# Performance work log

Measured on AMD Instinct MI355X. Metric: run time of the kernel, lower is better.

## Reference

```python
import jax, jax.numpy as jnp
import numpy as np


def _lstm_layer(x, W_ih, W_hh, b_ih, b_hh):
    """Single LSTM layer, batch_first input x: (B, T, in). PyTorch gate order i,f,g,o.
    Returns (full hidden sequence (B,T,H), final hidden (B,H))."""
    B = x.shape[0]
    H = W_hh.shape[1]
    # Precompute input projections for all timesteps (one big GEMM).
    x_proj = jnp.einsum('bti,gi->btg', x, W_ih) + (b_ih + b_hh)  # (B, T, 4H)
    x_proj = jnp.swapaxes(x_proj, 0, 1)  # (T, B, 4H) for scan
    h0 = jnp.zeros((B, H), x.dtype)
    c0 = jnp.zeros((B, H), x.dtype)

    def step(carry, xt):
        h, c = carry
        gates = xt + h @ W_hh.T  # (B, 4H)
        i, f, g, o = jnp.split(gates, 4, axis=-1)
        i = jax.nn.sigmoid(i)
        f = jax.nn.sigmoid(f)
        g = jnp.tanh(g)
        o = jax.nn.sigmoid(o)
        c = f * c + i * g
        h = o * jnp.tanh(c)
        return (h, c), h

    (hT, cT), hs = jax.lax.scan(step, (h0, c0), x_proj)
    return jnp.swapaxes(hs, 0, 1), hT  # (B,T,H), (B,H)


def setup_inputs() -> dict:
    key = jax.random.key(0)
    ks = jax.random.split(key, 9)
    B, T, I, H = 512, 2048, 3, 64
    s = 1.0 / float(np.sqrt(H))  # PyTorch LSTM init: U(-1/sqrt(H), 1/sqrt(H))

    def u(k, shape):
        return jax.random.uniform(k, shape, jnp.float32, -s, s)

    return {
        'x': jax.random.normal(ks[0], (B, T, I), jnp.float32),
        'W_ih0': u(ks[1], (4 * H, I)),
        'W_hh0': u(ks[2], (4 * H, H)),
        'b_ih0': u(ks[3], (4 * H,)),
        'b_hh0': u(ks[4], (4 * H,)),
        'W_ih1': u(ks[5], (4 * H, H)),
        'W_hh1': u(ks[6], (4 * H, H)),
        'b_ih1': u(ks[7], (4 * H,)),
        'b_hh1': u(ks[8], (4 * H,)),
    }


def reference(x, W_ih0, W_hh0, b_ih0, b_hh0, W_ih1, W_hh1, b_ih1, b_hh1):
    # 2-layer LSTM; inter-layer dropout (p=0.2) is inactive in eval mode, so omitted
    # for deterministic correctness checking.
    h1_seq, _ = _lstm_layer(x, W_ih0, W_hh0, b_ih0, b_hh0)
    _, h2_final = _lstm_layer(h1_seq, W_ih1, W_hh1, b_ih1, b_hh1)
    return h2_final  # (B, H) == h_n[-1]
```

## Files before the change

kernel.cpp:

```cpp
#include <hip/hip_runtime.h>
#include <math.h>


typedef _Float16 half8 __attribute__((ext_vector_type(8)));
typedef float    f32x4 __attribute__((ext_vector_type(4)));

constexpr int TT = 2048;
constexpr int HSTR = 80;

#define LOG2E  1.44269504088896340736f
#define LOG2E2 2.88539008177792681472f

__device__ __forceinline__ float sig_p(float y) {
    return __builtin_amdgcn_rcpf(1.0f + __builtin_amdgcn_exp2f(-y));
}
__device__ __forceinline__ float tanh_p(float y) {
    return 1.0f - 2.0f * __builtin_amdgcn_rcpf(__builtin_amdgcn_exp2f(y) + 1.0f);
}
__device__ __forceinline__ float sel4(f32x4 v, int q) {
    float lo = (q & 1) ? v[1] : v[0];
    float hi = (q & 1) ? v[3] : v[2];
    return (q & 2) ? hi : lo;
}

__device__ __forceinline__ void lds_barrier() {
    __builtin_amdgcn_sched_barrier(0);
    asm volatile("s_waitcnt lgkmcnt(0)" ::: "memory");
    __builtin_amdgcn_s_barrier();
    __builtin_amdgcn_sched_barrier(0);
}

__global__ __launch_bounds__(512) void lstm2_fused(
    const float* __restrict__ x,
    const float* __restrict__ Wih0, const float* __restrict__ Whh0,
    const float* __restrict__ bih0, const float* __restrict__ bhh0,
    const float* __restrict__ Wih1, const float* __restrict__ Whh1,
    const float* __restrict__ bih1, const float* __restrict__ bhh1,
    float* __restrict__ out)
{
    __shared__ __align__(16) _Float16 h1a[2][4 * HSTR];
    __shared__ __align__(16) _Float16 h2a[2][4 * HSTR];

    const int tid  = threadIdx.x;
    const int lane = tid & 63;
    const int wid  = tid >> 6;
    const int quad = lane >> 4;
    const int l16  = lane & 15;
    const bool isL1 = (wid >= 4);
    const int col  = (wid & 3) * 16 + l16;

    for (int i = tid; i < 2 * 4 * HSTR; i += 512) {
        ((_Float16*)h1a)[i] = (_Float16)0.0f;
        ((_Float16*)h2a)[i] = (_Float16)0.0f;
    }

    half8 wA[4][2];
    half8 wB[4][2];
    f32x4 cbias[4];
    float wxa[4], wxb[4], wxc[4];
    #pragma unroll
    for (int c = 0; c < 4; ++c) {
        const int row = c * 64 + col;
        const float sc = (c == 2) ? LOG2E2 : LOG2E;
        if (!isL1) {
            #pragma unroll
            for (int f = 0; f < 2; ++f) {
                const float* p = Whh0 + (size_t)row * 64 + f * 32 + quad * 8;
                half8 h;
                #pragma unroll
                for (int u = 0; u < 8; ++u) h[u] = (_Float16)(p[u] * sc);
                wA[c][f] = h;
            }
            const float b = (bih0[row] + bhh0[row]) * sc;
            cbias[c] = f32x4{b, b, b, b};
            wxa[c] = Wih0[row*3+0] * sc;
            wxb[c] = Wih0[row*3+1] * sc;
            wxc[c] = Wih0[row*3+2] * sc;
        } else {
            #pragma unroll
            for (int f = 0; f < 2; ++f) {
                const float* p = Whh1 + (size_t)row * 64 + f * 32 + quad * 8;
                half8 h;
                #pragma unroll
                for (int u = 0; u < 8; ++u) h[u] = (_Float16)(p[u] * sc);
                wA[c][f] = h;
                const float* q = Wih1 + (size_t)row * 64 + f * 32 + quad * 8;
                half8 g;
                #pragma unroll
                for (int u = 0; u < 8; ++u) g[u] = (_Float16)(q[u] * sc);
                wB[c][f] = g;
            }
            const float b = (bih1[row] + bhh1[row]) * sc;
            cbias[c] = f32x4{b, b, b, b};
        }
    }

    const float* xq = x + (size_t)(blockIdx.x * 4 + quad) * TT * 3;
    float xn0 = 0.f, xn1 = 0.f, xn2 = 0.f;
    if (!isL1) { xn0 = xq[0]; xn1 = xq[1]; xn2 = xq[2]; }

    const f32x4 Z = {0.f, 0.f, 0.f, 0.f};
    float cst = 0.0f;

    f32x4 accQ[2][4];
    #pragma unroll
    for (int s = 0; s < 2; ++s)
        #pragma unroll
        for (int c = 0; c < 4; ++c) accQ[s][c] = Z;

    __syncthreads();

    for (int bt = 0; bt <= TT + 1; bt += 2) {
        #pragma unroll
        for (int sub = 0; sub < 2; ++sub) {
            const int it   = bt + sub;
            const int cur  = sub;
            const int prev = sub ^ 1;

            if (!isL1) {
                if (it < TT) {
                    const _Float16* hb = h1a[prev] + (l16 & 3) * HSTR + quad * 8;
                    half8 a0 = *(const half8*)hb;
                    half8 a1 = *(const half8*)(hb + 32);

                    const float x0 = xn0, x1 = xn1, x2 = xn2;
                    float xp0 = fmaf(wxa[0], x0, fmaf(wxb[0], x1, wxc[0] * x2));
                    float xp1 = fmaf(wxa[1], x0, fmaf(wxb[1], x1, wxc[1] * x2));
                    float xp2 = fmaf(wxa[2], x0, fmaf(wxb[2], x1, wxc[2] * x2));
                    float xp3 = fmaf(wxa[3], x0, fmaf(wxb[3], x1, wxc[3] * x2));
                    const int nt = (it + 1 < TT) ? it + 1 : TT - 1;
                    const float* np = xq + nt * 3;
                    xn0 = np[0]; xn1 = np[1]; xn2 = np[2];

                    f32x4 acc[4];
                    #pragma unroll
                    for (int c = 0; c < 4; ++c) {
                        f32x4 z = cbias[c];
                        z = __builtin_amdgcn_mfma_f32_16x16x32_f16(a0, wA[c][0], z, 0, 0, 0);
                        z = __builtin_amdgcn_mfma_f32_16x16x32_f16(a1, wA[c][1], z, 0, 0, 0);
                        acc[c] = z;
                    }
                    float pi = sel4(acc[0], quad) + xp0;
                    float pf = sel4(acc[1], quad) + xp1;
                    float pg = sel4(acc[2], quad) + xp2;
                    float po = sel4(acc[3], quad) + xp3;
                    float iv = sig_p(pi),  fv = sig_p(pf);
                    float gv = tanh_p(pg), ov = sig_p(po);
                    cst = fmaf(fv, cst, iv * gv);
                    float th = tanh_p(cst * LOG2E2);
                    h1a[cur][quad * HSTR + col] = (_Float16)(ov * th);
                }
            } else {
                const bool doG = (it >= 2);
                const bool doQ = (it >= 1 && it <= TT);

                half8 a2, a3, b0, b1;
                if (doG) {
                    const _Float16* hb2 = h2a[prev] + (l16 & 3) * HSTR + quad * 8;
                    a2 = *(const half8*)hb2;
                    a3 = *(const half8*)(hb2 + 32);
                }
                if (doQ) {
                    const _Float16* hb1 = h1a[prev] + (l16 & 3) * HSTR + quad * 8;
                    b0 = *(const half8*)hb1;
                    b1 = *(const half8*)(hb1 + 32);
                }

                float qp0, qp1, qp2, qp3;
                if (doG) {
                    qp0 = sel4(accQ[prev][0], quad);
                    qp1 = sel4(accQ[prev][1], quad);
                    qp2 = sel4(accQ[prev][2], quad);
                    qp3 = sel4(accQ[prev][3], quad);
                }

                f32x4 acc[4];
                if (doG) {
                    #pragma unroll
                    for (int c = 0; c < 4; ++c) {
                        f32x4 z = cbias[c];
                        z = __builtin_amdgcn_mfma_f32_16x16x32_f16(a2, wA[c][0], z, 0, 0, 0);
                        z = __builtin_amdgcn_mfma_f32_16x16x32_f16(a3, wA[c][1], z, 0, 0, 0);
                        acc[c] = z;
                    }
                }
                if (doQ) {
                    #pragma unroll
                    for (int c = 0; c < 4; ++c) {
                        f32x4 z = Z;
                        z = __builtin_amdgcn_mfma_f32_16x16x32_f16(b0, wB[c][0], z, 0, 0, 0);
                        z = __builtin_amdgcn_mfma_f32_16x16x32_f16(b1, wB[c][1], z, 0, 0, 0);
                        accQ[sub][c] = z;
                    }
                }

                if (doG) {
                    float pi = sel4(acc[0], quad) + qp0;
                    float pf = sel4(acc[1], quad) + qp1;
                    float pg = sel4(acc[2], quad) + qp2;
                    float po = sel4(acc[3], quad) + qp3;
                    float iv = sig_p(pi),  fv = sig_p(pf);
                    float gv = tanh_p(pg), ov = sig_p(po);
                    cst = fmaf(fv, cst, iv * gv);
                    float hv = ov * tanh_p(cst * LOG2E2);
                    h2a[cur][quad * HSTR + col] = (_Float16)hv;
                    if (it == TT + 1)
                        out[(size_t)(blockIdx.x * 4 + quad) * 64 + col] = hv;
                }
            }
            lds_barrier();
        }
    }
}

extern "C" void kernel_launch(void* const* d_in, const int* in_sizes, int n_in,
                              void* d_out, int out_size, void* d_ws, size_t ws_size,
                              hipStream_t stream) {
    const float* x    = (const float*)d_in[0];
    const float* Wih0 = (const float*)d_in[1];
    const float* Whh0 = (const float*)d_in[2];
    const float* bih0 = (const float*)d_in[3];
    const float* bhh0 = (const float*)d_in[4];
    const float* Wih1 = (const float*)d_in[5];
    const float* Whh1 = (const float*)d_in[6];
    const float* bih1 = (const float*)d_in[7];
    const float* bhh1 = (const float*)d_in[8];
    float* out = (float*)d_out;

    lstm2_fused<<<128, 512, 0, stream>>>(x, Wih0, Whh0, bih0, bhh0,
                                         Wih1, Whh1, bih1, bhh1, out);
}
```

Baseline: 941.8 us.

## Split layer-2 input projection across layer-1 and layer-2 waves

Layer-1 waves now compute the i and f gate slices of layer 2's input projection from their own fresh h1 and hand them to layer-2 waves through an LDS buffer. Layer-2 waves keep only the g and o slices. This evens out MFMA work between the two wave groups on the serial recurrence critical path. It costs extra LDS traffic, an extra iteration for layer-1 waves, and relies on the existing barriers for buffer ordering.

```diff
diff --git a/kernel.cpp b/kernel.cpp
--- a/kernel.cpp
+++ b/kernel.cpp
@@ -40,6 +40,7 @@
 {
     __shared__ __align__(16) _Float16 h1a[2][4 * HSTR];
     __shared__ __align__(16) _Float16 h2a[2][4 * HSTR];
+    __shared__ __align__(16) float4   pIbuf[2][2][64];
 
     const int tid  = threadIdx.x;
     const int lane = tid & 63;
@@ -55,7 +56,7 @@
     }
 
     half8 wA[4][2];
-    half8 wB[4][2];
+    half8 wP[2][2];
     f32x4 cbias[4];
     float wxa[4], wxb[4], wxc[4];
     #pragma unroll
@@ -76,6 +77,16 @@
             wxa[c] = Wih0[row*3+0] * sc;
             wxb[c] = Wih0[row*3+1] * sc;
             wxc[c] = Wih0[row*3+2] * sc;
+            if (c < 2) {
+                #pragma unroll
+                for (int f = 0; f < 2; ++f) {
+                    const float* q = Wih1 + (size_t)row * 64 + f * 32 + quad * 8;
+                    half8 g;
+                    #pragma unroll
+                    for (int u = 0; u < 8; ++u) g[u] = (_Float16)(q[u] * sc);
+                    wP[c][f] = g;
+                }
+            }
         } else {
             #pragma unroll
             for (int f = 0; f < 2; ++f) {
@@ -84,14 +95,19 @@
                 #pragma unroll
                 for (int u = 0; u < 8; ++u) h[u] = (_Float16)(p[u] * sc);
                 wA[c][f] = h;
-                const float* q = Wih1 + (size_t)row * 64 + f * 32 + quad * 8;
-                half8 g;
-                #pragma unroll
-                for (int u = 0; u < 8; ++u) g[u] = (_Float16)(q[u] * sc);
-                wB[c][f] = g;
             }
             const float b = (bih1[row] + bhh1[row]) * sc;
             cbias[c] = f32x4{b, b, b, b};
+            if (c >= 2) {
+                #pragma unroll
+                for (int f = 0; f < 2; ++f) {
+                    const float* q = Wih1 + (size_t)row * 64 + f * 32 + quad * 8;
+                    half8 g;
+                    #pragma unroll
+                    for (int u = 0; u < 8; ++u) g[u] = (_Float16)(q[u] * sc);
+                    wP[c - 2][f] = g;
+                }
+            }
         }
     }
 
@@ -102,11 +118,11 @@
     const f32x4 Z = {0.f, 0.f, 0.f, 0.f};
     float cst = 0.0f;
 
-    f32x4 accQ[2][4];
+    f32x4 accQ[2][2];
     #pragma unroll
-    for (int s = 0; s < 2; ++s)
-        #pragma unroll
-        for (int c = 0; c < 4; ++c) accQ[s][c] = Z;
+    for (int s = 0; s < 2; ++s) {
+        accQ[s][0] = Z; accQ[s][1] = Z;
+    }
 
     __syncthreads();
 
@@ -118,37 +134,63 @@
             const int prev = sub ^ 1;
 
             if (!isL1) {
-                if (it < TT) {
+                if (it <= TT) {
                     const _Float16* hb = h1a[prev] + (l16 & 3) * HSTR + quad * 8;
                     half8 a0 = *(const half8*)hb;
                     half8 a1 = *(const half8*)(hb + 32);
 
-                    const float x0 = xn0, x1 = xn1, x2 = xn2;
-                    float xp0 = fmaf(wxa[0], x0, fmaf(wxb[0], x1, wxc[0] * x2));
-                    float xp1 = fmaf(wxa[1], x0, fmaf(wxb[1], x1, wxc[1] * x2));
-                    float xp2 = fmaf(wxa[2], x0, fmaf(wxb[2], x1, wxc[2] * x2));
-                    float xp3 = fmaf(wxa[3], x0, fmaf(wxb[3], x1, wxc[3] * x2));
-                    const int nt = (it + 1 < TT) ? it + 1 : TT - 1;
-                    const float* np = xq + nt * 3;
-                    xn0 = np[0]; xn1 = np[1]; xn2 = np[2];
+                    const bool doGate = (it < TT);
+                    const bool doP    = (it >= 1);
 
                     f32x4 acc[4];
-                    #pragma unroll
-                    for (int c = 0; c < 4; ++c) {
-                        f32x4 z = cbias[c];
-                        z = __builtin_amdgcn_mfma_f32_16x16x32_f16(a0, wA[c][0], z, 0, 0, 0);
-                        z = __builtin_amdgcn_mfma_f32_16x16x32_f16(a1, wA[c][1], z, 0, 0, 0);
-                        acc[c] = z;
-                    }
-                    float pi = sel4(acc[0], quad) + xp0;
-                    float pf = sel4(acc[1], quad) + xp1;
-                    float pg = sel4(acc[2], quad) + xp2;
-                    float po = sel4(acc[3], quad) + xp3;
-                    float iv = sig_p(pi),  fv = sig_p(pf);
-                    float gv = tanh_p(pg), ov = sig_p(po);
-                    cst = fmaf(fv, cst, iv * gv);
-                    float th = tanh_p(cst * LOG2E2);
-                    h1a[cur][quad * HSTR + col] = (_Float16)(ov * th);
+                    float xp0, xp1, xp2, xp3;
+                    if (doGate) {
+                        const float x0 = xn0, x1 = xn1, x2 = xn2;
+                        xp0 = fmaf(wxa[0], x0, fmaf(wxb[0], x1, wxc[0] * x2));
+                        xp1 = fmaf(wxa[1], x0, fmaf(wxb[1], x1, wxc[1] * x2));
+                        xp2 = fmaf(wxa[2], x0, fmaf(wxb[2], x1, wxc[2] * x2));
+                        xp3 = fmaf(wxa[3], x0, fmaf(wxb[3], x1, wxc[3] * x2));
+                        const int nt = (it + 1 < TT) ? it + 1 : TT - 1;
+                        const float* np = xq + nt * 3;
+                        xn0 = np[0]; xn1 = np[1]; xn2 = np[2];
+
+                        #pragma unroll
+                        for (int c = 0; c < 4; ++c) {
+                            f32x4 z = cbias[c];
+                            z = __builtin_amdgcn_mfma_f32_16x16x32_f16(a0, wA[c][0], z, 0, 0, 0);
+                            z = __builtin_amdgcn_mfma_f32_16x16x32_f16(a1, wA[c][1], z, 0, 0, 0);
+                            acc[c] = z;
+                        }
+                    }
+
+                    f32x4 accP0, accP1;
+                    if (doP) {
+                        f32x4 z0 = Z, z1 = Z;
+                        z0 = __builtin_amdgcn_mfma_f32_16x16x32_f16(a0, wP[0][0], z0, 0, 0, 0);
+                        z0 = __builtin_amdgcn_mfma_f32_16x16x32_f16(a1, wP[0][1], z0, 0, 0, 0);
+                        z1 = __builtin_amdgcn_mfma_f32_16x16x32_f16(a0, wP[1][0], z1, 0, 0, 0);
+                        z1 = __builtin_amdgcn_mfma_f32_16x16x32_f16(a1, wP[1][1], z1, 0, 0, 0);
+                        accP0 = z0; accP1 = z1;
+                    }
+
+                    if (doGate) {
+                        float pi = sel4(acc[0], quad) + xp0;
+                        float pf = sel4(acc[1], quad) + xp1;
+                        float pg = sel4(acc[2], quad) + xp2;
+                        float po = sel4(acc[3], quad) + xp3;
+                        float iv = sig_p(pi),  fv = sig_p(pf);
+                        float gv = tanh_p(pg), ov = sig_p(po);
+                        cst = fmaf(fv, cst, iv * gv);
+                        float th = tanh_p(cst * LOG2E2);
+                        h1a[cur][quad * HSTR + col] = (_Float16)(ov * th);
+                    }
+
+                    if (doP && quad == 0) {
+                        pIbuf[prev][0][col] = make_float4(accP0[0], accP0[1],
+                                                          accP0[2], accP0[3]);
+                        pIbuf[prev][1][col] = make_float4(accP1[0], accP1[1],
+                                                          accP1[2], accP1[3]);
+                    }
                 }
             } else {
                 const bool doG = (it >= 2);
@@ -168,10 +210,11 @@
 
                 float qp0, qp1, qp2, qp3;
                 if (doG) {
-                    qp0 = sel4(accQ[prev][0], quad);
-                    qp1 = sel4(accQ[prev][1], quad);
-                    qp2 = sel4(accQ[prev][2], quad);
-                    qp3 = sel4(accQ[prev][3], quad);
+                    const float* pb = (const float*)&pIbuf[cur][0][col] + quad;
+                    qp0 = pb[0];
+                    qp1 = pb[256];
+                    qp2 = sel4(accQ[prev][0], quad);
+                    qp3 = sel4(accQ[prev][1], quad);
                 }
 
                 f32x4 acc[4];
@@ -185,13 +228,13 @@
                     }
                 }
                 if (doQ) {
-                    #pragma unroll
-                    for (int c = 0; c < 4; ++c) {
-                        f32x4 z = Z;
-                        z = __builtin_amdgcn_mfma_f32_16x16x32_f16(b0, wB[c][0], z, 0, 0, 0);
-                        z = __builtin_amdgcn_mfma_f32_16x16x32_f16(b1, wB[c][1], z, 0, 0, 0);
-                        accQ[sub][c] = z;
-                    }
+                    f32x4 z2 = Z, z3 = Z;
+                    z2 = __builtin_amdgcn_mfma_f32_16x16x32_f16(b0, wP[0][0], z2, 0, 0, 0);
+                    z2 = __builtin_amdgcn_mfma_f32_16x16x32_f16(b1, wP[0][1], z2, 0, 0, 0);
+                    z3 = __builtin_amdgcn_mfma_f32_16x16x32_f16(b0, wP[1][0], z3, 0, 0, 0);
+                    z3 = __builtin_amdgcn_mfma_f32_16x16x32_f16(b1, wP[1][1], z3, 0, 0, 0);
+                    accQ[sub][0] = z2;
+                    accQ[sub][1] = z3;
                 }
 
                 if (doG) {
```

After: 978.2 us. +3.9%, slower.
